# Kernel optimization log

Measured on AMD Instinct MI355X. Metric: run time of the kernel, lower is better.

Reference implementation:

```python
import jax, jax.numpy as jnp
import numpy as np

B, N, F_IN, F_OUT, E = 2, 20000, 256, 256, 640000


def setup_inputs() -> dict:
    key = jax.random.key(0)
    k1, k2, k3, k4, k5, k6 = jax.random.split(key, 6)
    x = jax.random.normal(k1, (B, N, F_IN), dtype=jnp.float32)
    edge_index = jax.random.randint(k2, (2, E), 0, N, dtype=jnp.int64)
    s = 1.0 / np.sqrt(F_IN)
    W_l = jax.random.normal(k3, (F_OUT, F_IN), dtype=jnp.float32) * s
    b_l = jax.random.normal(k4, (F_OUT,), dtype=jnp.float32) * s
    W_r = jax.random.normal(k5, (F_OUT, F_IN), dtype=jnp.float32) * s
    return {"x": x, "edge_index": edge_index, "W_l": W_l, "b_l": b_l, "W_r": W_r}


def reference(x, edge_index, W_l, b_l, W_r):
    # PyG SAGEConv (mean aggr): out = lin_l(mean_{j in N(i)} x_j) + lin_r(x_i), ReLU on top.
    src = edge_index[0]  # message sources (x_j)
    tgt = edge_index[1]  # aggregation targets (i)
    n = x.shape[1]
    # gather messages: [B,E,F] -> [E,B,F] so segment axis is leading
    msgs = jnp.transpose(x[:, src, :], (1, 0, 2))
    agg = jax.ops.segment_sum(msgs, tgt, num_segments=n)  # [N,B,F]
    deg = jax.ops.segment_sum(jnp.ones((tgt.shape[0],), dtype=x.dtype), tgt, num_segments=n)
    agg = agg / jnp.maximum(deg, 1.0)[:, None, None]
    agg = jnp.transpose(agg, (1, 0, 2))  # [B,N,F]
    out = jnp.einsum('bnf,of->bno', agg, W_l) + b_l + jnp.einsum('bnf,of->bno', x, W_r)
    return jax.nn.relu(out)
```

## Files before the change

### kernel.cpp

```cpp
#include <hip/hip_runtime.h>

#define F 256
#define CAP 96

typedef short short8 __attribute__((ext_vector_type(8)));
typedef float floatx4 __attribute__((ext_vector_type(4)));
typedef float floatx2 __attribute__((ext_vector_type(2)));
typedef unsigned short u16;
typedef unsigned int u32;

__device__ __forceinline__ u16 f2bf(float f) {
    u32 u = __float_as_uint(f);
    u += 0x7fffu + ((u >> 16) & 1u);
    return (u16)(u >> 16);
}
__device__ __forceinline__ u32 pack2bf(float lo, float hi) {
    return (u32)f2bf(lo) | ((u32)f2bf(hi) << 16);
}

__device__ __forceinline__ void async16(const u16* g, u16* l) {
    __builtin_amdgcn_global_load_lds(
        (const __attribute__((address_space(1))) u32*)g,
        (__attribute__((address_space(3))) u32*)l, 16, 0, 0);
}

__global__ __launch_bounds__(256) void cast_hist_fill(
    const float* __restrict__ x, u16* __restrict__ xb, u32* __restrict__ xf8,
    int nx4,
    const float* __restrict__ Wl, u16* __restrict__ Wlb,
    const float* __restrict__ Wr, u16* __restrict__ Wrb, int nw4,
    const int* __restrict__ src, const int* __restrict__ tgt,
    int* __restrict__ count, u16* __restrict__ sorted, int E)
{
    int b = blockIdx.x;
    const int xblocks = nx4 >> 8;
    const int wblocks = nw4 >> 8;
    const int eblocks = (E + 255) >> 8;
    if (b < eblocks) {
        const int e = b * 256 + threadIdx.x;
        if (e >= E) return;
        const int t = tgt[e];
        const int s = src[e];
        const int rank = atomicAdd(&count[t], 1);
        if (rank < CAP) sorted[t * CAP + rank] = (u16)s;
        return;
    }
    b -= eblocks;
    if (b < xblocks) {
        const int idx = b * 256 + threadIdx.x;
        const float4 v = ((const float4*)x)[idx];
        ushort4 o;
        o.x = f2bf(v.x); o.y = f2bf(v.y); o.z = f2bf(v.z); o.w = f2bf(v.w);
        ((ushort4*)xb)[idx] = o;
        u32 p = __builtin_amdgcn_cvt_pk_fp8_f32(v.x, v.y, 0, false);
        p = __builtin_amdgcn_cvt_pk_fp8_f32(v.z, v.w, p, true);
        xf8[idx] = p;
        return;
    }
    b -= xblocks;
    {
        const float* s = (b < wblocks) ? Wl : Wr;
        u16* dst = (b < wblocks) ? Wlb : Wrb;
        if (b >= wblocks) b -= wblocks;
        const int idx = b * 256 + threadIdx.x;
        const float4 v = ((const float4*)s)[idx];
        ushort4 o;
        o.x = f2bf(v.x); o.y = f2bf(v.y); o.z = f2bf(v.z); o.w = f2bf(v.w);
        ((ushort4*)dst)[idx] = o;
    }
}

__global__ __launch_bounds__(256) void aggregate_kernel(
    const u32* __restrict__ xf8, const int* __restrict__ count,
    const u16* __restrict__ sorted, u16* __restrict__ aggb, int N)
{
    const int node = blockIdx.x * 4 + (threadIdx.x >> 6);
    if (node >= N) return;
    const int l = threadIdx.x & 63;
    const int bsel = l >> 5;
    const int l32 = l & 31;
    const int cnt = count[node];
    const int end = min(cnt, CAP);
    const u16* edges = sorted + node * CAP;

    const u32* base = xf8 + (size_t)bsel * N * 64 + l32 * 2;

    floatx2 a0 = {0, 0}, a1 = {0, 0}, a2 = {0, 0}, a3 = {0, 0};
    int e = 0;
    for (; e + 8 <= end; e += 8) {
        uint2 u[8];
        #pragma unroll
        for (int i = 0; i < 8; ++i)
            u[i] = *(const uint2*)(base + (size_t)edges[e + i] * 64);
        #pragma unroll
        for (int i = 0; i < 8; ++i) {
            a0 += __builtin_amdgcn_cvt_pk_f32_fp8(u[i].x, false);
            a1 += __builtin_amdgcn_cvt_pk_f32_fp8(u[i].x, true);
            a2 += __builtin_amdgcn_cvt_pk_f32_fp8(u[i].y, false);
            a3 += __builtin_amdgcn_cvt_pk_f32_fp8(u[i].y, true);
        }
    }
    for (; e < end; ++e) {
        const uint2 u0 = *(const uint2*)(base + (size_t)edges[e] * 64);
        a0 += __builtin_amdgcn_cvt_pk_f32_fp8(u0.x, false);
        a1 += __builtin_amdgcn_cvt_pk_f32_fp8(u0.x, true);
        a2 += __builtin_amdgcn_cvt_pk_f32_fp8(u0.y, false);
        a3 += __builtin_amdgcn_cvt_pk_f32_fp8(u0.y, true);
    }

    const float inv = 1.0f / fmaxf((float)cnt, 1.0f);
    uint4 o;
    o.x = pack2bf(a0.x * inv, a0.y * inv);
    o.y = pack2bf(a1.x * inv, a1.y * inv);
    o.z = pack2bf(a2.x * inv, a2.y * inv);
    o.w = pack2bf(a3.x * inv, a3.y * inv);
    *(uint4*)((u32*)(aggb + (size_t)bsel * N * F) + (size_t)node * 128 + l32 * 4) = o;
}

__global__ __launch_bounds__(256) void gemm_mfma(
    const u16* __restrict__ aggb, const u16* __restrict__ xb,
    const u16* __restrict__ Wlb, const u16* __restrict__ Wrb,
    const float* __restrict__ bl, float* __restrict__ out)
{
    __shared__ u16 ldsA[64 * 32];
    __shared__ u16 ldsB[256 * 32];

    const int tid = threadIdx.x;
    const int w = tid >> 6;
    const int l = tid & 63;
    const int m0 = blockIdx.x * 64;

    const int srow = tid >> 2;
    const int sslot = (tid & 3) ^ ((tid >> 3) & 3);

    floatx4 acc[4][4] = {};

    for (int kc = 0; kc < 16; ++kc) {
        const bool first = kc < 8;
        const int k0 = (first ? kc : kc - 8) * 32;
        const u16* A = first ? aggb : xb;
        const u16* B = first ? Wlb : Wrb;

        async16(A + (size_t)(m0 + srow) * F + k0 + sslot * 8,
                &ldsA[w * 512]);
        #pragma unroll
        for (int j = 0; j < 4; ++j)
            async16(B + (size_t)(j * 64 + srow) * F + k0 + sslot * 8,
                    &ldsB[j * 2048 + w * 512]);
        __syncthreads();

        const int sl = l >> 4;
        const int rkey = ((l & 15) >> 1) & 3;
        const int poff = (sl ^ rkey) * 8;
        short8 af[4], bfr[4];
        #pragma unroll
        for (int i = 0; i < 4; ++i)
            af[i] = *(const short8*)&ldsA[(i * 16 + (l & 15)) * 32 + poff];
        #pragma unroll
        for (int j = 0; j < 4; ++j)
            bfr[j] = *(const short8*)&ldsB[(w * 64 + j * 16 + (l & 15)) * 32 + poff];
        #pragma unroll
        for (int i = 0; i < 4; ++i)
            #pragma unroll
            for (int j = 0; j < 4; ++j)
                acc[i][j] = __builtin_amdgcn_mfma_f32_16x16x32_bf16(
                    af[i], bfr[j], acc[i][j], 0, 0, 0);
        __syncthreads();
    }

    #pragma unroll
    for (int j = 0; j < 4; ++j) {
        const int col = w * 64 + j * 16 + (l & 15);
        const float bias = bl[col];
        #pragma unroll
        for (int i = 0; i < 4; ++i) {
            const int rbase = m0 + i * 16 + (l >> 4) * 4;
            #pragma unroll
            for (int r = 0; r < 4; ++r)
                out[(size_t)(rbase + r) * F + col] = fmaxf(acc[i][j][r] + bias, 0.0f);
        }
    }
}

extern "C" void kernel_launch(void* const* d_in, const int* in_sizes, int n_in,
                              void* d_out, int out_size, void* d_ws, size_t ws_size,
                              hipStream_t stream)
{
    const float* x  = (const float*)d_in[0];
    const int*   ei = (const int*)d_in[1];
    const float* Wl = (const float*)d_in[2];
    const float* bl = (const float*)d_in[3];
    const float* Wr = (const float*)d_in[4];
    float* out = (float*)d_out;

    const int E = in_sizes[1] / 2;
    const int N = in_sizes[0] / (2 * F);
    const int M = 2 * N;

    const int* src = ei;
    const int* tgt = ei + E;

    int* count  = (int*)d_ws;
    u16* sorted = (u16*)(count + N);
    u16* xb     = sorted + (size_t)N * CAP;
    u16* aggb   = xb + (size_t)M * F;
    u16* Wlb    = aggb + (size_t)M * F;
    u16* Wrb    = Wlb + F * F;
    u32* xf8    = (u32*)(Wrb + F * F);

    hipMemsetAsync(count, 0, (size_t)N * sizeof(int), stream);

    const int nx4 = M * F / 4;
    const int nw4 = F * F / 4;
    const int eblocks = (E + 255) / 256;
    const int total_blocks = eblocks + nx4 / 256 + 2 * (nw4 / 256);
    cast_hist_fill<<<total_blocks, 256, 0, stream>>>(
        x, xb, xf8, nx4, Wl, Wlb, Wr, Wrb, nw4, src, tgt, count, sorted, E);

    aggregate_kernel<<<(N + 3) / 4, 256, 0, stream>>>(xf8, count, sorted, aggb, N);

    gemm_mfma<<<M / 64, 256, 0, stream>>>(aggb, xb, Wlb, Wrb, bl, out);
}
```

Baseline: 194.7 us.

## Partition edge bucketing per XCD to avoid cross-die atomic contention

The edge histogram/fill now keeps a separate count and bucket array per XCC (read via the hardware XCC_ID register), so atomics from different dies hit disjoint memory instead of the same counters. The aggregation kernel merges the eight per-die sublists into an LDS edge list before gathering, and uses the summed true count for the mean. This is meant to cut cross-die coherence traffic on the atomics. In exchange it adds an 8x larger count memset, extra reads during the merge, and a per-die cap of 24 edges that can drop edges when one die sees a skewed share. It also relies on an LDS write followed by reads from other lanes with no barrier.

```diff
diff --git a/kernel.cpp b/kernel.cpp
--- a/kernel.cpp
+++ b/kernel.cpp
@@ -1,7 +1,8 @@
 #include <hip/hip_runtime.h>
 
 #define F 256
-#define CAP 96
+#define SCAP 24
+#define ELCAP 192
 
 typedef short short8 __attribute__((ext_vector_type(8)));
 typedef float floatx4 __attribute__((ext_vector_type(4)));
@@ -22,6 +23,12 @@
     __builtin_amdgcn_global_load_lds(
         (const __attribute__((address_space(1))) u32*)g,
         (__attribute__((address_space(3))) u32*)l, 16, 0, 0);
+}
+
+__device__ __forceinline__ int xcc_id() {
+    int x;
+    asm volatile("s_getreg_b32 %0, hwreg(HW_REG_XCC_ID)" : "=s"(x));
+    return x & 7;
 }
 
 __global__ __launch_bounds__(256) void cast_hist_fill(
@@ -30,7 +37,7 @@
     const float* __restrict__ Wl, u16* __restrict__ Wlb,
     const float* __restrict__ Wr, u16* __restrict__ Wrb, int nw4,
     const int* __restrict__ src, const int* __restrict__ tgt,
-    int* __restrict__ count, u16* __restrict__ sorted, int E)
+    int* __restrict__ count8, u16* __restrict__ sorted8, int E, int N)
 {
     int b = blockIdx.x;
     const int xblocks = nx4 >> 8;
@@ -39,10 +46,11 @@
     if (b < eblocks) {
         const int e = b * 256 + threadIdx.x;
         if (e >= E) return;
+        const int xcd = xcc_id();
         const int t = tgt[e];
         const int s = src[e];
-        const int rank = atomicAdd(&count[t], 1);
-        if (rank < CAP) sorted[t * CAP + rank] = (u16)s;
+        const int rank = atomicAdd(&count8[xcd * N + t], 1);
+        if (rank < SCAP) sorted8[(size_t)(xcd * N + t) * SCAP + rank] = (u16)s;
         return;
     }
     b -= eblocks;
@@ -71,17 +79,30 @@
 }
 
 __global__ __launch_bounds__(256) void aggregate_kernel(
-    const u32* __restrict__ xf8, const int* __restrict__ count,
-    const u16* __restrict__ sorted, u16* __restrict__ aggb, int N)
-{
+    const u32* __restrict__ xf8, const int* __restrict__ count8,
+    const u16* __restrict__ sorted8, u16* __restrict__ aggb, int N)
+{
+    __shared__ u16 elist_s[4][ELCAP];
     const int node = blockIdx.x * 4 + (threadIdx.x >> 6);
     if (node >= N) return;
+    const int wid = threadIdx.x >> 6;
+    u16* elist = elist_s[wid];
     const int l = threadIdx.x & 63;
     const int bsel = l >> 5;
     const int l32 = l & 31;
-    const int cnt = count[node];
-    const int end = min(cnt, CAP);
-    const u16* edges = sorted + node * CAP;
+
+    int total = 0, truecnt = 0;
+    #pragma unroll
+    for (int s = 0; s < 8; ++s) {
+        const int c = count8[s * N + node];
+        int take = min(c, SCAP);
+        take = min(take, ELCAP - total);
+        if (l < take)
+            elist[total + l] = sorted8[(size_t)(s * N + node) * SCAP + l];
+        total += take;
+        truecnt += c;
+    }
+    const int end = total;
 
     const u32* base = xf8 + (size_t)bsel * N * 64 + l32 * 2;
 
@@ -91,7 +112,7 @@
         uint2 u[8];
         #pragma unroll
         for (int i = 0; i < 8; ++i)
-            u[i] = *(const uint2*)(base + (size_t)edges[e + i] * 64);
+            u[i] = *(const uint2*)(base + (size_t)elist[e + i] * 64);
         #pragma unroll
         for (int i = 0; i < 8; ++i) {
             a0 += __builtin_amdgcn_cvt_pk_f32_fp8(u[i].x, false);
@@ -101,14 +122,14 @@
         }
     }
     for (; e < end; ++e) {
-        const uint2 u0 = *(const uint2*)(base + (size_t)edges[e] * 64);
+        const uint2 u0 = *(const uint2*)(base + (size_t)elist[e] * 64);
         a0 += __builtin_amdgcn_cvt_pk_f32_fp8(u0.x, false);
         a1 += __builtin_amdgcn_cvt_pk_f32_fp8(u0.x, true);
         a2 += __builtin_amdgcn_cvt_pk_f32_fp8(u0.y, false);
         a3 += __builtin_amdgcn_cvt_pk_f32_fp8(u0.y, true);
     }
 
-    const float inv = 1.0f / fmaxf((float)cnt, 1.0f);
+    const float inv = 1.0f / fmaxf((float)truecnt, 1.0f);
     uint4 o;
     o.x = pack2bf(a0.x * inv, a0.y * inv);
     o.y = pack2bf(a1.x * inv, a1.y * inv);
@@ -200,24 +221,24 @@
     const int* src = ei;
     const int* tgt = ei + E;
 
-    int* count  = (int*)d_ws;
-    u16* sorted = (u16*)(count + N);
-    u16* xb     = sorted + (size_t)N * CAP;
-    u16* aggb   = xb + (size_t)M * F;
-    u16* Wlb    = aggb + (size_t)M * F;
-    u16* Wrb    = Wlb + F * F;
-    u32* xf8    = (u32*)(Wrb + F * F);
-
-    hipMemsetAsync(count, 0, (size_t)N * sizeof(int), stream);
+    int* count8  = (int*)d_ws;
+    u16* sorted8 = (u16*)(count8 + 8 * (size_t)N);
+    u16* xb      = sorted8 + (size_t)8 * N * SCAP;
+    u16* aggb    = xb + (size_t)M * F;
+    u16* Wlb     = aggb + (size_t)M * F;
+    u16* Wrb     = Wlb + F * F;
+    u32* xf8     = (u32*)(Wrb + F * F);
+
+    hipMemsetAsync(count8, 0, (size_t)8 * N * sizeof(int), stream);
 
     const int nx4 = M * F / 4;
     const int nw4 = F * F / 4;
     const int eblocks = (E + 255) / 256;
     const int total_blocks = eblocks + nx4 / 256 + 2 * (nw4 / 256);
     cast_hist_fill<<<total_blocks, 256, 0, stream>>>(
-        x, xb, xf8, nx4, Wl, Wlb, Wr, Wrb, nw4, src, tgt, count, sorted, E);
-
-    aggregate_kernel<<<(N + 3) / 4, 256, 0, stream>>>(xf8, count, sorted, aggb, N);
+        x, xb, xf8, nx4, Wl, Wlb, Wr, Wrb, nw4, src, tgt, count8, sorted8, E, N);
+
+    aggregate_kernel<<<(N + 3) / 4, 256, 0, stream>>>(xf8, count8, sorted8, aggb, N);
 
     gemm_mfma<<<M / 64, 256, 0, stream>>>(aggb, xb, Wlb, Wrb, bl, out);
 }
```

Measured after the change: 196.0 us. Within noise of the previous version (+0.6%).
